# Optimization experiments

Hardware: AMD Instinct MI355X
Metric: run time of the kernel (lower is better)

## Reference

```python
import jax, jax.numpy as jnp
import numpy as np

E = 1024
H = 16
D = E // H
S = 2048
B = 2

def setup_inputs() -> dict:
    key = jax.random.key(0)
    ks = jax.random.split(key, 5)
    x = jax.random.normal(ks[0], (B, S, E), dtype=jnp.float32)
    W_qkv = jax.random.normal(ks[1], (E, 3 * E), dtype=jnp.float32) / np.sqrt(E)
    b_qkv = jax.random.normal(ks[2], (3 * E,), dtype=jnp.float32) * 0.02
    W_out = jax.random.normal(ks[3], (E, E), dtype=jnp.float32) / np.sqrt(E)
    b_out = jax.random.normal(ks[4], (E,), dtype=jnp.float32) * 0.02
    return {"x": x, "W_qkv": W_qkv, "b_qkv": b_qkv, "W_out": W_out, "b_out": b_out}

def reference(x, W_qkv, b_qkv, W_out, b_out):
    b, s, e = x.shape
    qkv = x @ W_qkv + b_qkv                      # [B,S,3E]
    q, k, v = jnp.split(qkv, 3, axis=-1)
    # [B,S,E] -> [B,H,S,D]
    q = q.reshape(b, s, H, D).transpose(0, 2, 1, 3)
    k = k.reshape(b, s, H, D).transpose(0, 2, 1, 3)
    v = v.reshape(b, s, H, D).transpose(0, 2, 1, 3)
    scale = 1.0 / np.sqrt(D)
    att = jnp.einsum('bhqd,bhkd->bhqk', q, k) * scale
    causal = jnp.tril(jnp.ones((s, s), dtype=bool))
    att = jnp.where(causal[None, None], att, -jnp.inf)
    att = jax.nn.softmax(att, axis=-1)
    out = jnp.einsum('bhqk,bhkd->bhqd', att, v)  # [B,H,S,D]
    out = out.transpose(0, 2, 1, 3).reshape(b, s, e)
    return out @ W_out + b_out
```

## Files before the change

kernel.cpp:

```cpp
#include <hip/hip_runtime.h>

typedef unsigned short u16;
typedef __bf16  bf16x8 __attribute__((ext_vector_type(8)));
typedef float   f32x4  __attribute__((ext_vector_type(4)));
typedef unsigned int   u32x4 __attribute__((ext_vector_type(4)));
typedef unsigned short u16x4 __attribute__((ext_vector_type(4)));
typedef unsigned short u16x8 __attribute__((ext_vector_type(8)));

#define BB 2
#define HH 16
#define DD 64
#define SS 2048
#define EE 1024

#define QSCALE 0.1803368801111244f

static __device__ __forceinline__ u16 f2bf(float f) {
    unsigned int u = __float_as_uint(f);
    u += 0x7FFFu + ((u >> 16) & 1u);
    return (u16)(u >> 16);
}

union BfCast { u32x4 u; bf16x8 b; };
static __device__ __forceinline__ bf16x8 ldb8(const u16* p) {
    BfCast x; x.u = *(const u32x4*)p; return x.b;
}

static __device__ __forceinline__ void gload16(const u16* g, u16* l) {
    __builtin_amdgcn_global_load_lds(
        (const __attribute__((address_space(1))) unsigned int*)g,
        (__attribute__((address_space(3))) unsigned int*)l, 16, 0, 0);
}

#define UG (32 * 512)
static __device__ __forceinline__ int kidx(int s, int d) {
    return (((s >> 4) * 2 + (d >> 5)) * 512) + ((((d >> 3) & 3) * 16 + (s & 15)) * 8) + (d & 7);
}
static __device__ __forceinline__ int vidx(int key, int d) {
    return (((key >> 5) * 4 + (d >> 4)) * 512) + ((((key >> 3) & 3) * 16 + (d & 15)) * 8) + (key & 7);
}

__global__ __launch_bounds__(256) void prep_kernel(
    const float* __restrict__ x,    u16* __restrict__ xb,
    const float* __restrict__ Wqkv, u16* __restrict__ wqkvT,
    const float* __restrict__ Wout, u16* __restrict__ woutT)
{
    __shared__ float tile[32][33];
    const int bid = blockIdx.x;
    if (bid < 2048) {
        const int t = bid * 256 + threadIdx.x;
        const int u = t >> 6, w = t & 63;
        const int m = (u >> 5) * 16 + (w & 15);
        const int k = (u & 31) * 32 + (w >> 4) * 8;
        const float* p = x + m * 1024 + k;
        const f32x4 a = *(const f32x4*)p;
        const f32x4 b = *(const f32x4*)(p + 4);
        u16x8 o;
        o[0] = f2bf(a[0]); o[1] = f2bf(a[1]); o[2] = f2bf(a[2]); o[3] = f2bf(a[3]);
        o[4] = f2bf(b[0]); o[5] = f2bf(b[1]); o[6] = f2bf(b[2]); o[7] = f2bf(b[3]);
        *(u16x8*)&xb[u * 512 + w * 8] = o;
        return;
    }
    const float* in; u16* out; int C, tb;
    if (bid < 2048 + 3072) { in = Wqkv; out = wqkvT; C = 3072; tb = bid - 2048; }
    else                   { in = Wout; out = woutT; C = 1024; tb = bid - 5120; }
    const int tx = threadIdx.x & 31;
    const int ty = threadIdx.x >> 5;
    const int ct = C >> 5;
    const int bc = tb % ct, br = tb / ct;
    const int c0 = bc * 32, r0 = br * 32;
    #pragma unroll
    for (int i = 0; i < 4; i++)
        tile[ty + i * 8][tx] = in[(r0 + ty + i * 8) * C + c0 + tx];
    __syncthreads();
    #pragma unroll
    for (int i = 0; i < 4; i++) {
        const int n = c0 + ty + i * 8;
        out[((n >> 4) * 32 + (r0 >> 5)) * 512 + (((tx >> 3) & 3) * 16 + (n & 15)) * 8 + (tx & 7)]
            = f2bf(tile[tx][ty + i * 8]);
    }
}

__global__ __launch_bounds__(256) void gemm_qkv_kernel(
    const u16* __restrict__ Af,
    const u16* __restrict__ Bf,
    const float* __restrict__ bias,
    u16* __restrict__ Qb, u16* __restrict__ Kb, u16* __restrict__ Vb)
{
    __shared__ __align__(16) u16 Us[2][16 * 512];
    const int lane = threadIdx.x & 63;
    const int wave = threadIdx.x >> 6;
    const int nb = 3 * EE / 128;
    const int tm = blockIdx.x / nb, tn = blockIdx.x % nb;
    const int lm = lane & 15, quad = lane >> 4;

    const u16* sp[4];
    #pragma unroll
    for (int j = 0; j < 4; j++) {
        const int idx = 4 * wave + j;
        sp[j] = (idx < 8) ? (Af + (tm * 8 + idx) * UG + lane * 8)
                          : (Bf + (tn * 8 + idx - 8) * UG + lane * 8);
    }
    u16* ld0 = &Us[0][4 * wave * 512];
    u16* ld1 = &Us[1][4 * wave * 512];

    const int wy = wave >> 1, wx = wave & 1;
    f32x4 acc[4][4] = {};

    #pragma unroll
    for (int j = 0; j < 4; j++) gload16(sp[j], ld0 + j * 512);

    for (int it = 0; it < 32; ++it) {
        const int cur = it & 1;
        __syncthreads();
        if (it + 1 < 32) {
            u16* ld = cur ? ld0 : ld1;
            const int ko = (it + 1) * 512;
            #pragma unroll
            for (int j = 0; j < 4; j++) gload16(sp[j] + ko, ld + j * 512);
        }
        bf16x8 af[4], bf[4];
        #pragma unroll
        for (int i = 0; i < 4; i++) {
            af[i] = ldb8(&Us[cur][(wy * 4 + i) * 512 + lane * 8]);
            bf[i] = ldb8(&Us[cur][(8 + wx * 4 + i) * 512 + lane * 8]);
        }
        #pragma unroll
        for (int mi = 0; mi < 4; mi++)
            #pragma unroll
            for (int ni = 0; ni < 4; ni++)
                acc[mi][ni] = __builtin_amdgcn_mfma_f32_16x16x32_bf16(af[mi], bf[ni], acc[mi][ni], 0, 0, 0);
    }

    const int gm0 = tm * 128 + wy * 64;
    const int gn0 = tn * 128 + wx * 64;
    #pragma unroll
    for (int ni = 0; ni < 4; ni++) {
        const int n = gn0 + ni * 16 + lm;
        const float bv = bias[n];
        const int which = n >> 10;
        const int e = n & 1023;
        const int h = e >> 6, d = e & 63;
        #pragma unroll
        for (int mi = 0; mi < 4; mi++) {
            if (which == 2) {
                const int m0 = gm0 + mi * 16 + quad * 4;
                const int b = m0 >> 11, key0 = m0 & 2047;
                u16x4 pk;
                #pragma unroll
                for (int r = 0; r < 4; r++) pk[r] = f2bf(acc[mi][ni][r] + bv);
                *(u16x4*)&Vb[(b * HH + h) * 131072 + vidx(key0, d)] = pk;
            } else if (which == 1) {
                #pragma unroll
                for (int r = 0; r < 4; r++) {
                    const int m = gm0 + mi * 16 + quad * 4 + r;
                    const int b = m >> 11, s = m & 2047;
                    Kb[(b * HH + h) * 131072 + kidx(s, d)] = f2bf(acc[mi][ni][r] + bv);
                }
            } else {
                #pragma unroll
                for (int r = 0; r < 4; r++) {
                    const int m = gm0 + mi * 16 + quad * 4 + r;
                    const int b = m >> 11, s = m & 2047;
                    Qb[((b * HH + h) * SS + s) * DD + d] = f2bf((acc[mi][ni][r] + bv) * QSCALE);
                }
            }
        }
    }
}

__global__ __launch_bounds__(256) void attn_kernel(
    const u16* __restrict__ Qb, const u16* __restrict__ Kb,
    const u16* __restrict__ Vb, u16* __restrict__ Ob)
{
    __shared__ __align__(16) u16 Ks[2][4096];
    __shared__ __align__(16) u16 Vs[2][4096];
    __shared__ __align__(16) u16 Plds[4 * 16 * 72];
    const int tid = threadIdx.x;
    const int lane = tid & 63, wave = tid >> 6;
    const int lm = lane & 15, quad = lane >> 4;
    const int bh = blockIdx.x & 31;
    const int qt = (SS / 128 - 1) - (blockIdx.x >> 5);
    const int q0 = qt * 128;
    const int qrow = q0 + wave * 32;
    const int b = bh >> 4, h = bh & 15;

    const u16* qbase = Qb + (bh * SS + qrow) * DD;
    bf16x8 qf[2][2];
    #pragma unroll
    for (int f = 0; f < 2; f++) {
        qf[f][0] = ldb8(qbase + (f * 16 + lm) * DD + quad * 8);
        qf[f][1] = ldb8(qbase + (f * 16 + lm) * DD + 32 + quad * 8);
    }

    const u16* ktile = Kb + bh * 131072;
    const u16* vtile = Vb + bh * 131072;
    u16* Pw = Plds + wave * (16 * 72);

    BfCast oc; oc.u = (u32x4){0x3F803F80u, 0x3F803F80u, 0x3F803F80u, 0x3F803F80u};
    const bf16x8 ones = oc.b;

    f32x4 oacc[2][4] = {};
    f32x4 lacc[2] = {};

    const int ktmax = qt * 2 + 2;
    {
        const u16* kg = ktile + wave * 1024 + lane * 8;
        const u16* vg = vtile + wave * 1024 + lane * 8;
        gload16(kg,       &Ks[0][wave * 1024]);
        gload16(kg + 512, &Ks[0][wave * 1024 + 512]);
        gload16(vg,       &Vs[0][wave * 1024]);
        gload16(vg + 512, &Vs[0][wave * 1024 + 512]);
    }
    for (int kt = 0; kt < ktmax; ++kt) {
        const int cur = kt & 1;
        const int k0 = kt * 64;
        __syncthreads();
        if (kt + 1 < ktmax) {
            const u16* kg = ktile + (kt + 1) * 4096 + wave * 1024 + lane * 8;
            const u16* vg = vtile + (kt + 1) * 4096 + wave * 1024 + lane * 8;
            gload16(kg,       &Ks[cur ^ 1][wave * 1024]);
            gload16(kg + 512, &Ks[cur ^ 1][wave * 1024 + 512]);
            gload16(vg,       &Vs[cur ^ 1][wave * 1024]);
            gload16(vg + 512, &Vs[cur ^ 1][wave * 1024 + 512]);
        }

        #pragma unroll
        for (int f = 0; f < 2; f++) {
            const int qrf = qrow + f * 16;
            if (k0 > qrf + 15) continue;

            f32x4 s[4];
            #pragma unroll
            for (int g = 0; g < 4; g++) {
                f32x4 z = {0.f, 0.f, 0.f, 0.f};
                z    = __builtin_amdgcn_mfma_f32_16x16x32_bf16(ldb8(&Ks[cur][(g * 2) * 512 + lane * 8]), qf[f][0], z, 0, 0, 0);
                s[g] = __builtin_amdgcn_mfma_f32_16x16x32_bf16(ldb8(&Ks[cur][(g * 2 + 1) * 512 + lane * 8]), qf[f][1], z, 0, 0, 0);
            }
            if (k0 + 63 > qrf) {
                const int lim = qrf + lm - k0 - quad * 4;
                #pragma unroll
                for (int g = 0; g < 4; g++)
                    #pragma unroll
                    for (int r = 0; r < 4; r++)
                        if (g * 16 + r > lim) s[g][r] = -INFINITY;
            }
            #pragma unroll
            for (int g = 0; g < 4; g++) {
                u16x4 pk;
                #pragma unroll
                for (int r = 0; r < 4; r++) pk[r] = f2bf(__builtin_amdgcn_exp2f(s[g][r]));
                *(u16x4*)&Pw[lm * 72 + g * 16 + quad * 4] = pk;
            }
            const bf16x8 pf0 = ldb8(&Pw[lm * 72 + quad * 8]);
            const bf16x8 pf1 = ldb8(&Pw[lm * 72 + 32 + quad * 8]);
            lacc[f] = __builtin_amdgcn_mfma_f32_16x16x32_bf16(ones, pf0, lacc[f], 0, 0, 0);
            lacc[f] = __builtin_amdgcn_mfma_f32_16x16x32_bf16(ones, pf1, lacc[f], 0, 0, 0);
            #pragma unroll
            for (int dg = 0; dg < 4; dg++) {
                oacc[f][dg] = __builtin_amdgcn_mfma_f32_16x16x32_bf16(ldb8(&Vs[cur][dg * 512 + lane * 8]), pf0, oacc[f][dg], 0, 0, 0);
                oacc[f][dg] = __builtin_amdgcn_mfma_f32_16x16x32_bf16(ldb8(&Vs[cur][(4 + dg) * 512 + lane * 8]), pf1, oacc[f][dg], 0, 0, 0);
            }
        }
    }
    #pragma unroll
    for (int f = 0; f < 2; f++) {
        const float inv = 1.0f / lacc[f][0];
        u16* ob = Ob + (((b * SS + qrow + f * 16) >> 4) * 32 + h * 2) * 512;
        #pragma unroll
        for (int dg = 0; dg < 4; dg++) {
            u16x4 pk;
            #pragma unroll
            for (int r = 0; r < 4; r++) pk[r] = f2bf(oacc[f][dg][r] * inv);
            *(u16x4*)&ob[(dg >> 1) * 512 + (((dg * 2 + (quad >> 1)) & 3) * 16 + lm) * 8 + (quad & 1) * 4] = pk;
        }
    }
}

__global__ __launch_bounds__(256) void gemm_out_kernel(
    const u16* __restrict__ Af,
    const u16* __restrict__ Bf,
    const float* __restrict__ bias,
    float* __restrict__ Out)
{
    __shared__ __align__(16) u16 Us[2][16 * 512];
    const int lane = threadIdx.x & 63;
    const int wave = threadIdx.x >> 6;
    const int nb = EE / 128;
    const int tm = blockIdx.x / nb, tn = blockIdx.x % nb;
    const int lm = lane & 15, quad = lane >> 4;

    const u16* sp[4];
    #pragma unroll
    for (int j = 0; j < 4; j++) {
        const int idx = 4 * wave + j;
        sp[j] = (idx < 8) ? (Af + (tm * 8 + idx) * UG + lane * 8)
                          : (Bf + (tn * 8 + idx - 8) * UG + lane * 8);
    }
    u16* ld0 = &Us[0][4 * wave * 512];
    u16* ld1 = &Us[1][4 * wave * 512];

    const int wy = wave >> 1, wx = wave & 1;
    f32x4 acc[4][4] = {};

    #pragma unroll
    for (int j = 0; j < 4; j++) gload16(sp[j], ld0 + j * 512);

    for (int it = 0; it < 32; ++it) {
        const int cur = it & 1;
        __syncthreads();
        if (it + 1 < 32) {
            u16* ld = cur ? ld0 : ld1;
            const int ko = (it + 1) * 512;
            #pragma unroll
            for (int j = 0; j < 4; j++) gload16(sp[j] + ko, ld + j * 512);
        }
        bf16x8 af[4], bf[4];
        #pragma unroll
        for (int i = 0; i < 4; i++) {
            af[i] = ldb8(&Us[cur][(wy * 4 + i) * 512 + lane * 8]);
            bf[i] = ldb8(&Us[cur][(8 + wx * 4 + i) * 512 + lane * 8]);
        }
        #pragma unroll
        for (int mi = 0; mi < 4; mi++)
            #pragma unroll
            for (int ni = 0; ni < 4; ni++)
                acc[mi][ni] = __builtin_amdgcn_mfma_f32_16x16x32_bf16(af[mi], bf[ni], acc[mi][ni], 0, 0, 0);
    }

    const int gm0 = tm * 128 + wy * 64;
    const int gn0 = tn * 128 + wx * 64;
    #pragma unroll
    for (int ni = 0; ni < 4; ni++) {
        const int n = gn0 + ni * 16 + lm;
        const float bv = bias[n];
        #pragma unroll
        for (int mi = 0; mi < 4; mi++)
            #pragma unroll
            for (int r = 0; r < 4; r++)
                Out[(gm0 + mi * 16 + quad * 4 + r) * EE + n] = acc[mi][ni][r] + bv;
    }
}

extern "C" void kernel_launch(void* const* d_in, const int* in_sizes, int n_in,
                              void* d_out, int out_size, void* d_ws, size_t ws_size,
                              hipStream_t stream)
{
    const float* x     = (const float*)d_in[0];
    const float* Wqkv  = (const float*)d_in[1];
    const float* bqkv  = (const float*)d_in[2];
    const float* Wout  = (const float*)d_in[3];
    const float* bout  = (const float*)d_in[4];
    float* out = (float*)d_out;

    char* ws = (char*)d_ws;
    u16* xb    = (u16*)(ws + 0);
    u16* wqkvT = (u16*)(ws + 8388608);
    u16* woutT = (u16*)(ws + 14680064);
    u16* Qb    = (u16*)(ws + 16777216);
    u16* Kb    = (u16*)(ws + 25165824);
    u16* Vb    = (u16*)(ws + 33554432);
    u16* Ob    = (u16*)(ws + 41943040);
    if (ws_size < 50331648) return;

    prep_kernel<<<2048 + 3072 + 1024, 256, 0, stream>>>(x, xb, Wqkv, wqkvT, Wout, woutT);
    gemm_qkv_kernel<<<(BB * SS / 128) * (3 * EE / 128), 256, 0, stream>>>(xb, wqkvT, bqkv, Qb, Kb, Vb);
    attn_kernel<<<BB * HH * (SS / 128), 256, 0, stream>>>(Qb, Kb, Vb, Ob);
    gemm_out_kernel<<<(BB * SS / 128) * (EE / 128), 256, 0, stream>>>(Ob, woutT, bout, out);
}
```

Before: 188.0 us.

## Pair short and long causal query tiles per attention block for balanced work

Each attention block now handles two 64-row query tiles, one from the end and one from the start of the sequence (qtA = 31 - pr, qtB = pr), so causal work per block is roughly equal and K/V tiles loaded once feed both. K and V fragments are loaded into registers once per key tile and reused for both query tiles. Bf16 conversion switches to the hardware v_cvt_pk_bf16_f32 instruction in place of manual rounding. This adds register pressure, and the launch grid must match the new pairing (half as many blocks), which is not visible here.

```diff
diff --git a/kernel.cpp b/kernel.cpp
--- a/kernel.cpp
+++ b/kernel.cpp
@@ -3,6 +3,7 @@
 typedef unsigned short u16;
 typedef __bf16  bf16x8 __attribute__((ext_vector_type(8)));
 typedef float   f32x4  __attribute__((ext_vector_type(4)));
+typedef unsigned int   u32x2 __attribute__((ext_vector_type(2)));
 typedef unsigned int   u32x4 __attribute__((ext_vector_type(4)));
 typedef unsigned short u16x4 __attribute__((ext_vector_type(4)));
 typedef unsigned short u16x8 __attribute__((ext_vector_type(8)));
@@ -19,6 +20,12 @@
     unsigned int u = __float_as_uint(f);
     u += 0x7FFFu + ((u >> 16) & 1u);
     return (u16)(u >> 16);
+}
+
+static __device__ __forceinline__ unsigned int cvtpk(float lo, float hi) {
+    unsigned int r;
+    asm("v_cvt_pk_bf16_f32 %0, %1, %2" : "=v"(r) : "v"(lo), "v"(hi));
+    return r;
 }
 
 union BfCast { u32x4 u; bf16x8 b; };
@@ -180,18 +187,18 @@
     const int lane = tid & 63, wave = tid >> 6;
     const int lm = lane & 15, quad = lane >> 4;
     const int bh = blockIdx.x & 31;
-    const int qt = (SS / 128 - 1) - (blockIdx.x >> 5);
-    const int q0 = qt * 128;
-    const int qrow = q0 + wave * 32;
+    const int pr = blockIdx.x >> 5;
+    const int qtA = 31 - pr, qtB = pr;
+    const int qrowA = qtA * 64 + wave * 16;
+    const int qrowB = qtB * 64 + wave * 16;
     const int b = bh >> 4, h = bh & 15;
 
-    const u16* qbase = Qb + (bh * SS + qrow) * DD;
-    bf16x8 qf[2][2];
-    #pragma unroll
-    for (int f = 0; f < 2; f++) {
-        qf[f][0] = ldb8(qbase + (f * 16 + lm) * DD + quad * 8);
-        qf[f][1] = ldb8(qbase + (f * 16 + lm) * DD + 32 + quad * 8);
-    }
+    const u16* qbaseA = Qb + (bh * SS + qrowA) * DD;
+    const u16* qbaseB = Qb + (bh * SS + qrowB) * DD;
+    const bf16x8 qfA0 = ldb8(qbaseA + lm * DD + quad * 8);
+    const bf16x8 qfA1 = ldb8(qbaseA + lm * DD + 32 + quad * 8);
+    const bf16x8 qfB0 = ldb8(qbaseB + lm * DD + quad * 8);
+    const bf16x8 qfB1 = ldb8(qbaseB + lm * DD + 32 + quad * 8);
 
     const u16* ktile = Kb + bh * 131072;
     const u16* vtile = Vb + bh * 131072;
@@ -200,10 +207,11 @@
     BfCast oc; oc.u = (u32x4){0x3F803F80u, 0x3F803F80u, 0x3F803F80u, 0x3F803F80u};
     const bf16x8 ones = oc.b;
 
-    f32x4 oacc[2][4] = {};
-    f32x4 lacc[2] = {};
-
-    const int ktmax = qt * 2 + 2;
+    f32x4 oaccA[4] = {}, oaccB[4] = {};
+    f32x4 laccA = {0.f, 0.f, 0.f, 0.f};
+    f32x4 laccB = {0.f, 0.f, 0.f, 0.f};
+
+    const int ktmax = qtA + 1;
     {
         const u16* kg = ktile + wave * 1024 + lane * 8;
         const u16* vg = vtile + wave * 1024 + lane * 8;
@@ -225,54 +233,106 @@
             gload16(vg + 512, &Vs[cur ^ 1][wave * 1024 + 512]);
         }
 
-        #pragma unroll
-        for (int f = 0; f < 2; f++) {
-            const int qrf = qrow + f * 16;
-            if (k0 > qrf + 15) continue;
-
-            f32x4 s[4];
+        const bool doB = (kt <= qtB);
+
+        bf16x8 kf[8];
+        #pragma unroll
+        for (int u = 0; u < 8; u++) kf[u] = ldb8(&Ks[cur][u * 512 + lane * 8]);
+
+        f32x4 sA[4], sB[4];
+        #pragma unroll
+        for (int g = 0; g < 4; g++) {
+            f32x4 z = {0.f, 0.f, 0.f, 0.f};
+            z     = __builtin_amdgcn_mfma_f32_16x16x32_bf16(kf[g * 2],     qfA0, z, 0, 0, 0);
+            sA[g] = __builtin_amdgcn_mfma_f32_16x16x32_bf16(kf[g * 2 + 1], qfA1, z, 0, 0, 0);
+        }
+        if (doB) {
             #pragma unroll
             for (int g = 0; g < 4; g++) {
                 f32x4 z = {0.f, 0.f, 0.f, 0.f};
-                z    = __builtin_amdgcn_mfma_f32_16x16x32_bf16(ldb8(&Ks[cur][(g * 2) * 512 + lane * 8]), qf[f][0], z, 0, 0, 0);
-                s[g] = __builtin_amdgcn_mfma_f32_16x16x32_bf16(ldb8(&Ks[cur][(g * 2 + 1) * 512 + lane * 8]), qf[f][1], z, 0, 0, 0);
+                z     = __builtin_amdgcn_mfma_f32_16x16x32_bf16(kf[g * 2],     qfB0, z, 0, 0, 0);
+                sB[g] = __builtin_amdgcn_mfma_f32_16x16x32_bf16(kf[g * 2 + 1], qfB1, z, 0, 0, 0);
             }
-            if (k0 + 63 > qrf) {
-                const int lim = qrf + lm - k0 - quad * 4;
+        }
+
+        if (k0 + 63 > qrowA) {
+            const int lim = qrowA + lm - k0 - quad * 4;
+            #pragma unroll
+            for (int g = 0; g < 4; g++)
                 #pragma unroll
-                for (int g = 0; g < 4; g++)
-                    #pragma unroll
-                    for (int r = 0; r < 4; r++)
-                        if (g * 16 + r > lim) s[g][r] = -INFINITY;
+                for (int r = 0; r < 4; r++)
+                    if (g * 16 + r > lim) sA[g][r] = -INFINITY;
+        }
+        if (doB && (k0 + 63 > qrowB)) {
+            const int lim = qrowB + lm - k0 - quad * 4;
+            #pragma unroll
+            for (int g = 0; g < 4; g++)
+                #pragma unroll
+                for (int r = 0; r < 4; r++)
+                    if (g * 16 + r > lim) sB[g][r] = -INFINITY;
+        }
+
+        bf16x8 vf[8];
+        #pragma unroll
+        for (int u = 0; u < 8; u++) vf[u] = ldb8(&Vs[cur][u * 512 + lane * 8]);
+
+        #pragma unroll
+        for (int g = 0; g < 4; g++) {
+            u32x2 w;
+            w[0] = cvtpk(__builtin_amdgcn_exp2f(sA[g][0]), __builtin_amdgcn_exp2f(sA[g][1]));
+            w[1] = cvtpk(__builtin_amdgcn_exp2f(sA[g][2]), __builtin_amdgcn_exp2f(sA[g][3]));
+            *(u32x2*)&Pw[lm * 72 + g * 16 + quad * 4] = w;
+        }
+        const bf16x8 pfA0 = ldb8(&Pw[lm * 72 + quad * 8]);
+        const bf16x8 pfA1 = ldb8(&Pw[lm * 72 + 32 + quad * 8]);
+        laccA = __builtin_amdgcn_mfma_f32_16x16x32_bf16(ones, pfA0, laccA, 0, 0, 0);
+        laccA = __builtin_amdgcn_mfma_f32_16x16x32_bf16(ones, pfA1, laccA, 0, 0, 0);
+        #pragma unroll
+        for (int dg = 0; dg < 4; dg++) {
+            oaccA[dg] = __builtin_amdgcn_mfma_f32_16x16x32_bf16(vf[dg],     pfA0, oaccA[dg], 0, 0, 0);
+            oaccA[dg] = __builtin_amdgcn_mfma_f32_16x16x32_bf16(vf[4 + dg], pfA1, oaccA[dg], 0, 0, 0);
+        }
+
+        if (doB) {
+            #pragma unroll
+            for (int g = 0; g < 4; g++) {
+                u32x2 w;
+                w[0] = cvtpk(__builtin_amdgcn_exp2f(sB[g][0]), __builtin_amdgcn_exp2f(sB[g][1]));
+                w[1] = cvtpk(__builtin_amdgcn_exp2f(sB[g][2]), __builtin_amdgcn_exp2f(sB[g][3]));
+                *(u32x2*)&Pw[lm * 72 + g * 16 + quad * 4] = w;
             }
-            #pragma unroll
-            for (int g = 0; g < 4; g++) {
-                u16x4 pk;
-                #pragma unroll
-                for (int r = 0; r < 4; r++) pk[r] = f2bf(__builtin_amdgcn_exp2f(s[g][r]));
-                *(u16x4*)&Pw[lm * 72 + g * 16 + quad * 4] = pk;
+            const bf16x8 pfB0 = ldb8(&Pw[lm * 72 + quad * 8]);
+            const bf16x8 pfB1 = ldb8(&Pw[lm * 72 + 32 + quad * 8]);
+            laccB = __builtin_amdgcn_mfma_f32_16x16x32_bf16(ones, pfB0, laccB, 0, 0, 0);
+            laccB = __builtin_amdgcn_mfma_f32_16x16x32_bf16(ones, pfB1, laccB, 0, 0, 0);
+            #pragma unroll
+            for (int dg = 0; dg < 4; dg++) {
+                oaccB[dg] = __builtin_amdgcn_mfma_f32_16x16x32_bf16(vf[dg],     pfB0, oaccB[dg], 0, 0, 0);
+                oaccB[dg] = __builtin_amdgcn_mfma_f32_16x16x32_bf16(vf[4 + dg], pfB1, oaccB[dg], 0, 0, 0);
             }
-            const bf16x8 pf0 = ldb8(&Pw[lm * 72 + quad * 8]);
-            const bf16x8 pf1 = ldb8(&Pw[lm * 72 + 32 + quad * 8]);
-            lacc[f] = __builtin_amdgcn_mfma_f32_16x16x32_bf16(ones, pf0, lacc[f], 0, 0, 0);
-            lacc[f] = __builtin_amdgcn_mfma_f32_16x16x32_bf16(ones, pf1, lacc[f], 0, 0, 0);
-            #pragma unroll
-            for (int dg = 0; dg < 4; dg++) {
-                oacc[f][dg] = __builtin_amdgcn_mfma_f32_16x16x32_bf16(ldb8(&Vs[cur][dg * 512 + lane * 8]), pf0, oacc[f][dg], 0, 0, 0);
-                oacc[f][dg] = __builtin_amdgcn_mfma_f32_16x16x32_bf16(ldb8(&Vs[cur][(4 + dg) * 512 + lane * 8]), pf1, oacc[f][dg], 0, 0, 0);
-            }
-        }
-    }
-    #pragma unroll
-    for (int f = 0; f < 2; f++) {
-        const float inv = 1.0f / lacc[f][0];
-        u16* ob = Ob + (((b * SS + qrow + f * 16) >> 4) * 32 + h * 2) * 512;
+        }
+    }
+
+    {
+        const float inv = 1.0f / laccA[0];
+        u16* ob = Ob + (((b * SS + qrowA) >> 4) * 32 + h * 2) * 512;
         #pragma unroll
         for (int dg = 0; dg < 4; dg++) {
-            u16x4 pk;
-            #pragma unroll
-            for (int r = 0; r < 4; r++) pk[r] = f2bf(oacc[f][dg][r] * inv);
-            *(u16x4*)&ob[(dg >> 1) * 512 + (((dg * 2 + (quad >> 1)) & 3) * 16 + lm) * 8 + (quad & 1) * 4] = pk;
+            u32x2 w;
+            w[0] = cvtpk(oaccA[dg][0] * inv, oaccA[dg][1] * inv);
+            w[1] = cvtpk(oaccA[dg][2] * inv, oaccA[dg][3] * inv);
+            *(u32x2*)&ob[(dg >> 1) * 512 + (((dg * 2 + (quad >> 1)) & 3) * 16 + lm) * 8 + (quad & 1) * 4] = w;
+        }
+    }
+    {
+        const float inv = 1.0f / laccB[0];
+        u16* ob = Ob + (((b * SS + qrowB) >> 4) * 32 + h * 2) * 512;
+        #pragma unroll
+        for (int dg = 0; dg < 4; dg++) {
+            u32x2 w;
+            w[0] = cvtpk(oaccB[dg][0] * inv, oaccB[dg][1] * inv);
+            w[1] = cvtpk(oaccB[dg][2] * inv, oaccB[dg][3] * inv);
+            *(u32x2*)&ob[(dg >> 1) * 512 + (((dg * 2 + (quad >> 1)) & 3) * 16 + lm) * 8 + (quad & 1) * 4] = w;
         }
     }
 }
```

Result: faster. 174.5 us (-7.2%).
